# Kernel tuning notes

Measured on AMD Instinct MI355X. Metric: run time of the kernel, lower is better.

## Reference

```python
import jax, jax.numpy as jnp
import numpy as np

B, S, D = 4, 4096, 4096
N_EXPERTS = 64
TOP_K = 2
EPS = 1e-5


def setup_inputs() -> dict:
    key = jax.random.key(0)
    k1, k2 = jax.random.split(key)
    x = jax.random.normal(k1, (B, S, D), dtype=jnp.float32)
    # nn.Linear weight: [n_experts, input_dim], applied as x @ W.T
    gate_w = jax.random.normal(k2, (N_EXPERTS, D), dtype=jnp.float32) * (1.0 / np.sqrt(D))
    temperature = jnp.float32(1.0)
    return {"x": x, "gate_w": gate_w, "temperature": temperature}


def reference(x, gate_w, temperature):
    # gate projection: [B,S,D] @ [D,E] -> [B,S,E], scaled by |temp| + eps
    logits = jnp.einsum("bsd,ed->bse", x, gate_w) / (jnp.abs(temperature) + EPS)
    # top-k over experts
    top_vals, top_idx = jax.lax.top_k(logits, TOP_K)          # [B,S,k]
    routing_weights = jax.nn.softmax(top_vals, axis=-1)        # [B,S,k]
    # scatter weights into dense [B,S,E] routing matrix (one-hot sum; k is tiny)
    one_hot = jax.nn.one_hot(top_idx, N_EXPERTS, dtype=routing_weights.dtype)  # [B,S,k,E]
    routing_matrix = jnp.einsum("bsk,bske->bse", routing_weights, one_hot)
    return routing_matrix, top_idx
```

## Files before the change

### kernel.cpp

```cpp
#include <hip/hip_runtime.h>
#include <cstdint>
#include <cstddef>
#include <math.h>

#define TOKENS 16384
#define DIM    4096
#define NE     64
#define MT     128
#define KT     32
#define KT4    (KT/4)
#define X_F4   (MT*KT4)
#define W_F4   (NE*KT4)

static_assert(TOKENS % MT == 0, "tile");

__device__ __forceinline__ int swz(int row) { return (row >> 2) & 7; }

__device__ __forceinline__ void gload16(const void* g, void* l) {
  __builtin_amdgcn_global_load_lds(
      (const __attribute__((address_space(1))) void*)g,
      (__attribute__((address_space(3))) void*)l, 16, 0, 0);
}

__global__ __launch_bounds__(256, 1)
void dr_gemm(const float* __restrict__ x, const float* __restrict__ gw,
             float* __restrict__ p0, float* __restrict__ p1, int steps)
{
  __shared__ float4 xs4[2 * X_F4];
  __shared__ float4 ws4[2 * W_F4];

  const int t    = threadIdx.x;
  const int lane = t & 63;
  const int wv   = t >> 6;
  const int ng   = t & 15;
  const int mg   = t >> 4;

  const int bm    = blockIdx.x & 127;
  const int h     = blockIdx.x >> 7;
  const int kbase = h * steps * KT;
  float* __restrict__ dst = h ? p1 : p0;

  size_t xoff[4]; int xlds[4];
#pragma unroll
  for (int r = 0; r < 4; ++r) {
    int row = r * 32 + wv * 8 + (lane >> 3);
    int c4  = (lane & 7) ^ swz(row);
    xoff[r] = ((size_t)(bm * MT + row) * DIM + kbase + 4 * c4) * sizeof(float);
    xlds[r] = (r * 32 + wv * 8) * KT4;
  }
  size_t woff[2]; int wlds[2];
#pragma unroll
  for (int r = 0; r < 2; ++r) {
    int row = r * 32 + wv * 8 + (lane >> 3);
    int c4  = (lane & 7) ^ swz(row);
    woff[r] = ((size_t)row * DIM + kbase + 4 * c4) * sizeof(float);
    wlds[r] = (r * 32 + wv * 8) * KT4;
  }

  const char* xb = (const char*)x;
  const char* wb = (const char*)gw;

  auto stage = [&](int buf, int sidx) {
    size_t kb = (size_t)sidx * KT * sizeof(float);
#pragma unroll
    for (int r = 0; r < 4; ++r)
      gload16(xb + xoff[r] + kb, (void*)(xs4 + buf * X_F4 + xlds[r]));
#pragma unroll
    for (int r = 0; r < 2; ++r)
      gload16(wb + woff[r] + kb, (void*)(ws4 + buf * W_F4 + wlds[r]));
  };

  float acc[8][4], accl[8][4];
#pragma unroll
  for (int i = 0; i < 8; ++i)
#pragma unroll
    for (int j = 0; j < 4; ++j) { acc[i][j] = 0.f; accl[i][j] = 0.f; }

  stage(0, 0);
  __syncthreads();

  int buf = 0;
  for (int s = 0; s < steps; ++s) {
    if (s + 1 < steps) stage(buf ^ 1, s + 1);
    const float4* X = xs4 + buf * X_F4;
    const float4* W = ws4 + buf * W_F4;
#pragma unroll
    for (int c4 = 0; c4 < KT4; ++c4) {
      float4 bv[4];
#pragma unroll
      for (int j = 0; j < 4; ++j) {
        int row = 4 * ng + j;
        bv[j] = W[row * KT4 + (c4 ^ swz(row))];
      }
#pragma unroll
      for (int i = 0; i < 8; ++i) {
        int row = 8 * mg + i;
        float4 a = X[row * KT4 + (c4 ^ swz(row))];
#pragma unroll
        for (int j = 0; j < 4; ++j) {
          accl[i][j] = fmaf(a.x, bv[j].x, accl[i][j]);
          accl[i][j] = fmaf(a.y, bv[j].y, accl[i][j]);
          accl[i][j] = fmaf(a.z, bv[j].z, accl[i][j]);
          accl[i][j] = fmaf(a.w, bv[j].w, accl[i][j]);
        }
      }
    }
#pragma unroll
    for (int i = 0; i < 8; ++i)
#pragma unroll
      for (int j = 0; j < 4; ++j) { acc[i][j] += accl[i][j]; accl[i][j] = 0.f; }
    __syncthreads();
    buf ^= 1;
  }

#pragma unroll
  for (int i = 0; i < 8; ++i) {
    int row = bm * MT + 8 * mg + i;
    float4 v = make_float4(acc[i][0], acc[i][1], acc[i][2], acc[i][3]);
    reinterpret_cast<float4*>(dst)[(size_t)row * (NE / 4) + ng] = v;
  }
}

__global__ __launch_bounds__(256)
void dr_combine(const float* __restrict__ p0, const float* __restrict__ p1, int two,
                const float* __restrict__ temp, float* __restrict__ outr,
                float* __restrict__ outi)
{
  int tok = blockIdx.x * 4 + (threadIdx.x >> 6);
  int e   = threadIdx.x & 63;
  float invT = 1.0f / (fabsf(temp[0]) + 1e-5f);
  size_t base = (size_t)tok * NE + e;
  float v = p0[base];
  if (two) v += p1[base];
  v *= invT;

  float bv = v; int bi = e;
#pragma unroll
  for (int off = 32; off; off >>= 1) {
    float ov = __shfl_xor(bv, off);
    int   oi = __shfl_xor(bi, off);
    if (ov > bv || (ov == bv && oi < bi)) { bv = ov; bi = oi; }
  }
  float v0 = bv; int i0 = bi;

  float vm = (e == i0) ? -INFINITY : v;
  bv = vm; bi = e;
#pragma unroll
  for (int off = 32; off; off >>= 1) {
    float ov = __shfl_xor(bv, off);
    int   oi = __shfl_xor(bi, off);
    if (ov > bv || (ov == bv && oi < bi)) { bv = ov; bi = oi; }
  }
  float v1 = bv; int i1 = bi;

  float ed = expf(v1 - v0);
  float s  = 1.0f / (1.0f + ed);
  float w0 = s, w1 = ed * s;

  outr[base] = (e == i0) ? w0 : (e == i1) ? w1 : 0.0f;
  if (e == 0) {
    outi[(size_t)tok * 2]     = (float)i0;
    outi[(size_t)tok * 2 + 1] = (float)i1;
  }
}

extern "C" void kernel_launch(void* const* d_in, const int* in_sizes, int n_in,
                              void* d_out, int out_size, void* d_ws, size_t ws_size,
                              hipStream_t stream)
{
  const float* x  = (const float*)d_in[0];
  const float* gw = (const float*)d_in[1];
  const float* tp = (const float*)d_in[2];
  float* outr = (float*)d_out;
  float* outi = outr + (size_t)TOKENS * NE;
  float* p1   = (float*)d_ws;

  bool split = ws_size >= (size_t)TOKENS * NE * sizeof(float);
  if (split) {
    dr_gemm<<<dim3(256), dim3(256), 0, stream>>>(x, gw, outr, p1, 64);
    dr_combine<<<dim3(TOKENS / 4), dim3(256), 0, stream>>>(outr, p1, 1, tp, outr, outi);
  } else {
    dr_gemm<<<dim3(128), dim3(256), 0, stream>>>(x, gw, outr, (float*)nullptr, 128);
    dr_combine<<<dim3(TOKENS / 4), dim3(256), 0, stream>>>(outr, outr, 0, tp, outr, outi);
  }
}
```

Measured before the change: 480.5 us.

## Generalize split-K to up to eight parts and read gate weights from global

The K dimension is now split into up to eight partitions, chosen by available workspace, which raises the grid from 256 blocks to as many as 1024. The combine kernel sums all partial results. Gate-weight tiles are no longer staged in LDS; each thread reads its weight float4s directly from global memory, relying on cache. Launch bounds allow four blocks per CU and the per-step local accumulator is removed. Together these aim to improve occupancy and latency hiding, at the cost of more partial-sum traffic in the combine step and uncoalesced, cache-dependent weight loads.

Result: slower. 681.1 us (+41.7%).

```diff
diff --git a/kernel.cpp b/kernel.cpp
--- a/kernel.cpp
+++ b/kernel.cpp
@@ -10,7 +10,7 @@
 #define KT     32
 #define KT4    (KT/4)
 #define X_F4   (MT*KT4)
-#define W_F4   (NE*KT4)
+#define PART_ELEMS ((size_t)TOKENS * NE)
 
 static_assert(TOKENS % MT == 0, "tile");
 
@@ -22,12 +22,11 @@
       (__attribute__((address_space(3))) void*)l, 16, 0, 0);
 }
 
-__global__ __launch_bounds__(256, 1)
+__global__ __launch_bounds__(256, 4)
 void dr_gemm(const float* __restrict__ x, const float* __restrict__ gw,
-             float* __restrict__ p0, float* __restrict__ p1, int steps)
+             float* __restrict__ p0, float* __restrict__ pws, int steps)
 {
   __shared__ float4 xs4[2 * X_F4];
-  __shared__ float4 ws4[2 * W_F4];
 
   const int t    = threadIdx.x;
   const int lane = t & 63;
@@ -38,7 +37,7 @@
   const int bm    = blockIdx.x & 127;
   const int h     = blockIdx.x >> 7;
   const int kbase = h * steps * KT;
-  float* __restrict__ dst = h ? p1 : p0;
+  float* __restrict__ dst = h ? (pws + (size_t)(h - 1) * PART_ELEMS) : p0;
 
   size_t xoff[4]; int xlds[4];
 #pragma unroll
@@ -48,67 +47,52 @@
     xoff[r] = ((size_t)(bm * MT + row) * DIM + kbase + 4 * c4) * sizeof(float);
     xlds[r] = (r * 32 + wv * 8) * KT4;
   }
-  size_t woff[2]; int wlds[2];
-#pragma unroll
-  for (int r = 0; r < 2; ++r) {
-    int row = r * 32 + wv * 8 + (lane >> 3);
-    int c4  = (lane & 7) ^ swz(row);
-    woff[r] = ((size_t)row * DIM + kbase + 4 * c4) * sizeof(float);
-    wlds[r] = (r * 32 + wv * 8) * KT4;
-  }
-
   const char* xb = (const char*)x;
-  const char* wb = (const char*)gw;
 
   auto stage = [&](int buf, int sidx) {
     size_t kb = (size_t)sidx * KT * sizeof(float);
 #pragma unroll
     for (int r = 0; r < 4; ++r)
       gload16(xb + xoff[r] + kb, (void*)(xs4 + buf * X_F4 + xlds[r]));
-#pragma unroll
-    for (int r = 0; r < 2; ++r)
-      gload16(wb + woff[r] + kb, (void*)(ws4 + buf * W_F4 + wlds[r]));
   };
 
-  float acc[8][4], accl[8][4];
+  const float4* __restrict__ w4 = reinterpret_cast<const float4*>(gw)
+                                  + (size_t)(4 * ng) * (DIM / 4) + (kbase >> 2);
+
+  float acc[8][4];
 #pragma unroll
   for (int i = 0; i < 8; ++i)
 #pragma unroll
-    for (int j = 0; j < 4; ++j) { acc[i][j] = 0.f; accl[i][j] = 0.f; }
+    for (int j = 0; j < 4; ++j) acc[i][j] = 0.f;
 
   stage(0, 0);
   __syncthreads();
 
   int buf = 0;
+#pragma unroll 1
   for (int s = 0; s < steps; ++s) {
     if (s + 1 < steps) stage(buf ^ 1, s + 1);
-    const float4* X = xs4 + buf * X_F4;
-    const float4* W = ws4 + buf * W_F4;
+    const float4* X  = xs4 + buf * X_F4;
+    const float4* Wp = w4 + (size_t)s * KT4;
 #pragma unroll
     for (int c4 = 0; c4 < KT4; ++c4) {
       float4 bv[4];
 #pragma unroll
-      for (int j = 0; j < 4; ++j) {
-        int row = 4 * ng + j;
-        bv[j] = W[row * KT4 + (c4 ^ swz(row))];
-      }
+      for (int j = 0; j < 4; ++j)
+        bv[j] = Wp[(size_t)j * (DIM / 4) + c4];
 #pragma unroll
       for (int i = 0; i < 8; ++i) {
         int row = 8 * mg + i;
         float4 a = X[row * KT4 + (c4 ^ swz(row))];
 #pragma unroll
         for (int j = 0; j < 4; ++j) {
-          accl[i][j] = fmaf(a.x, bv[j].x, accl[i][j]);
-          accl[i][j] = fmaf(a.y, bv[j].y, accl[i][j]);
-          accl[i][j] = fmaf(a.z, bv[j].z, accl[i][j]);
-          accl[i][j] = fmaf(a.w, bv[j].w, accl[i][j]);
+          acc[i][j] = fmaf(a.x, bv[j].x, acc[i][j]);
+          acc[i][j] = fmaf(a.y, bv[j].y, acc[i][j]);
+          acc[i][j] = fmaf(a.z, bv[j].z, acc[i][j]);
+          acc[i][j] = fmaf(a.w, bv[j].w, acc[i][j]);
         }
       }
     }
-#pragma unroll
-    for (int i = 0; i < 8; ++i)
-#pragma unroll
-      for (int j = 0; j < 4; ++j) { acc[i][j] += accl[i][j]; accl[i][j] = 0.f; }
     __syncthreads();
     buf ^= 1;
   }
@@ -122,16 +106,18 @@
 }
 
 __global__ __launch_bounds__(256)
-void dr_combine(const float* __restrict__ p0, const float* __restrict__ p1, int two,
-                const float* __restrict__ temp, float* __restrict__ outr,
-                float* __restrict__ outi)
+void dr_combine(const float* __restrict__ p0, const float* __restrict__ pws,
+                int nparts, const float* __restrict__ temp,
+                float* __restrict__ outr, float* __restrict__ outi)
 {
   int tok = blockIdx.x * 4 + (threadIdx.x >> 6);
   int e   = threadIdx.x & 63;
   float invT = 1.0f / (fabsf(temp[0]) + 1e-5f);
   size_t base = (size_t)tok * NE + e;
+
   float v = p0[base];
-  if (two) v += p1[base];
+  for (int q = 1; q < nparts; ++q)
+    v += pws[(size_t)(q - 1) * PART_ELEMS + base];
   v *= invT;
 
   float bv = v; int bi = e;
@@ -172,15 +158,16 @@
   const float* gw = (const float*)d_in[1];
   const float* tp = (const float*)d_in[2];
   float* outr = (float*)d_out;
-  float* outi = outr + (size_t)TOKENS * NE;
-  float* p1   = (float*)d_ws;
+  float* outi = outr + PART_ELEMS;
 
-  bool split = ws_size >= (size_t)TOKENS * NE * sizeof(float);
-  if (split) {
-    dr_gemm<<<dim3(256), dim3(256), 0, stream>>>(x, gw, outr, p1, 64);
-    dr_combine<<<dim3(TOKENS / 4), dim3(256), 0, stream>>>(outr, p1, 1, tp, outr, outi);
-  } else {
-    dr_gemm<<<dim3(128), dim3(256), 0, stream>>>(x, gw, outr, (float*)nullptr, 128);
-    dr_combine<<<dim3(TOKENS / 4), dim3(256), 0, stream>>>(outr, outr, 0, tp, outr, outi);
-  }
+  const size_t part_bytes = PART_ELEMS * sizeof(float);
+  int split = 1;
+  if      (ws_size >= 7 * part_bytes) split = 8;
+  else if (ws_size >= 3 * part_bytes) split = 4;
+  else if (ws_size >= 1 * part_bytes) split = 2;
+  const int steps = 128 / split;
+
+  dr_gemm<<<dim3(128 * split), dim3(256), 0, stream>>>(x, gw, outr, (float*)d_ws, steps);
+  dr_combine<<<dim3(TOKENS / 4), dim3(256), 0, stream>>>(outr, (const float*)d_ws,
+                                                         split, tp, outr, outi);
 }
```
